# Kernel optimization log

Hardware: AMD Instinct MI355X
Metric: run time of the kernel (lower is better)

Reference implementation:

```python
import jax, jax.numpy as jnp
import numpy as np

B, S, D = 4, 4096, 64


def setup_inputs() -> dict:
    key = jax.random.key(0)
    ks = jax.random.split(key, 12)
    sc = 1.0 / np.sqrt(D)
    return {
        "q": jax.random.normal(ks[0], (B, S, D), jnp.float32),
        "k": jax.random.normal(ks[1], (B, S, D), jnp.float32),
        "v": jax.random.normal(ks[2], (B, S, D), jnp.float32),
        "attn_mask": jnp.ones((1, 1, 1), jnp.float32),
        "Wq": jax.random.normal(ks[3], (D, D), jnp.float32) * sc,
        "bq": jax.random.normal(ks[4], (D,), jnp.float32) * 0.01,
        "Wk": jax.random.normal(ks[5], (D, D), jnp.float32) * sc,
        "bk": jax.random.normal(ks[6], (D,), jnp.float32) * 0.01,
        "Wv": jax.random.normal(ks[7], (D, D), jnp.float32) * sc,
        "bv": jax.random.normal(ks[8], (D,), jnp.float32) * 0.01,
        "qw": jax.random.normal(ks[9], (1, 1, D), jnp.float32),
        "kw": jax.random.normal(ks[10], (1, 1, D), jnp.float32),
    }


def reference(q, k, v, attn_mask, Wq, bq, Wk, bk, Wv, bv, qw, kw):
    d = q.shape[-1]
    # Linear projections (torch Linear: x @ W.T + b)
    qp = q @ Wq.T + bq                      # (B,S,D)
    kp = k @ Wk.T + bk                      # (B,S,D)
    # learned per-feature elementwise weighting + 1/d scaling
    qwd = (qw * qp) / d                     # (B,S,D)
    kwd = (kw * kp) / d                     # (B,S,D)
    scores = jnp.einsum("bsd,btd->bst", qwd, kwd) + attn_mask  # (B,S,S)
    attn = jax.nn.softmax(scores, axis=-1)
    vp = v @ Wv.T + bv                      # (B,S,D)
    return jnp.einsum("bst,btd->bsd", attn, vp)
```

## Files before the change

### kernel.cpp

```cpp
#include <hip/hip_runtime.h>
#include <hip/hip_bf16.h>

typedef __attribute__((ext_vector_type(8)))  short    s16x8;
typedef __attribute__((ext_vector_type(16))) float    f32x16;
typedef __attribute__((ext_vector_type(4)))  unsigned u32x4;

#define NB 4
#define NS 4096
#define ND 64
#define NTOK (NB*NS)
#define PERB (NS*ND)

static __device__ __forceinline__ unsigned cvt_pk_bf16(float lo, float hi) {
    unsigned r;
    asm("v_cvt_pk_bf16_f32 %0, %1, %2" : "=v"(r) : "v"(lo), "v"(hi));
    return r;
}
static __device__ __forceinline__ float exp2_fast(float x) {
    float r;
    asm("v_exp_f32 %0, %1" : "=v"(r) : "v"(x));
    return r;
}
static __device__ __forceinline__ short f2bf_s(float x) {
    __hip_bfloat16 h = __float2bfloat16(x);
    return (short)__builtin_bit_cast(unsigned short, h);
}

__global__ __launch_bounds__(512) void proj_kernel(
    const float* __restrict__ q, const float* __restrict__ k, const float* __restrict__ v,
    const float* __restrict__ Wq, const float* __restrict__ bq,
    const float* __restrict__ Wk, const float* __restrict__ bk,
    const float* __restrict__ Wv, const float* __restrict__ bv,
    const float* __restrict__ qw, const float* __restrict__ kw,
    __hip_bfloat16* __restrict__ qf, __hip_bfloat16* __restrict__ kf,
    __hip_bfloat16* __restrict__ vf)
{
    const int which = blockIdx.y;
    const int wv    = __builtin_amdgcn_readfirstlane(threadIdx.x >> 6);
    const int lane  = threadIdx.x & 63;
    const int row   = blockIdx.x * 64 + lane;
    const float* X    = (which == 0) ? q  : (which == 1) ? k  : v;
    const float* W    = (which == 0) ? Wq : (which == 1) ? Wk : Wv;
    const float* bias = (which == 0) ? bq : (which == 1) ? bk : bv;

    float x[64];
    const float4* xr = (const float4*)(X + (size_t)row * ND);
    #pragma unroll
    for (int i = 0; i < 16; ++i) ((float4*)x)[i] = xr[i];

    float acc8[8];
    #pragma unroll
    for (int dd = 0; dd < 8; ++dd) {
        const float* wr = W + (8*wv + dd) * ND;
        float s = 0.f;
        #pragma unroll
        for (int i = 0; i < 64; ++i) s += x[i] * wr[i];
        acc8[dd] = s + bias[8*wv + dd];
    }

    const int b = row >> 12, t = row & (NS - 1);

    if (which == 2) {
        const size_t base = (size_t)b*PERB + (size_t)(t >> 6)*4096
                          + ((t >> 4) & 3)*512 + ((t >> 3) & 1)*256 + (t & 7)
                          + (wv >> 2)*2048;
        #pragma unroll
        for (int dd = 0; dd < 8; ++dd)
            vf[base + (8*(wv & 3) + dd)*8] = __float2bfloat16(acc8[dd]);
    } else {
        const float* sc = (which == 0) ? qw : kw;
        const float extra = (which == 0) ? 1.44269504088896f : 1.0f;
        s16x8 vch;
        #pragma unroll
        for (int j = 0; j < 8; ++j)
            vch[j] = f2bf_s(acc8[j] * sc[8*wv + j] * 0.015625f * extra);
        __hip_bfloat16* dst = ((which == 0) ? qf : kf)
            + (size_t)b*PERB + (size_t)(t >> 5)*2048 + wv*256 + (t & 31)*8;
        *(s16x8*)dst = vch;
    }
}

__global__ __launch_bounds__(64, 4) void attn_kernel(
    const __hip_bfloat16* __restrict__ qf, const __hip_bfloat16* __restrict__ kf,
    const __hip_bfloat16* __restrict__ vf,
    float* __restrict__ opart, float* __restrict__ lpart,
    float* __restrict__ outdirect, int nsplit)
{
    const int lane = threadIdx.x;
    const int r31 = lane & 31, hi = lane >> 5;
    const int bid = blockIdx.x;
    const int b     = bid & 3;
    const int qwi   = (bid >> 2) & 127;
    const int split = bid >> 9;

    const __hip_bfloat16* qb = qf + (size_t)b*PERB;
    const __hip_bfloat16* kb = kf + (size_t)b*PERB;
    const __hip_bfloat16* vb = vf + (size_t)b*PERB;

    const __hip_bfloat16* qr = qb + (size_t)qwi*2048 + hi*256 + r31*8;
    s16x8 bQ[4];
    #pragma unroll
    for (int c = 0; c < 4; ++c) bQ[c] = *(const s16x8*)(qr + c*512);

    f32x16 O0 = (f32x16)0.f, O1 = (f32x16)0.f;
    float l = 0.f;

    const int span  = NS / nsplit;
    const int tbeg  = split * span;
    const int iters = span >> 6;

    for (int it = 0; it < iters; ++it) {
        const int tb = tbeg + (it << 6);

        const __hip_bfloat16* kbase = kb + (size_t)(tb >> 5)*2048 + hi*256 + r31*8;
        f32x16 s0 = (f32x16)0.f, s1 = (f32x16)0.f;
        #pragma unroll
        for (int c = 0; c < 4; ++c) {
            s16x8 a0 = *(const s16x8*)(kbase + c*512);
            s16x8 a1 = *(const s16x8*)(kbase + 2048 + c*512);
            s0 = __builtin_amdgcn_mfma_f32_32x32x16_bf16(a0, bQ[c], s0, 0, 0, 0);
            s1 = __builtin_amdgcn_mfma_f32_32x32x16_bf16(a1, bQ[c], s1, 0, 0, 0);
        }

        #pragma unroll
        for (int r = 0; r < 16; ++r) { s0[r] = exp2_fast(s0[r]); s1[r] = exp2_fast(s1[r]); }
        float t0 = ((s0[0]+s0[1])+(s0[2]+s0[3])) + ((s0[4]+s0[5])+(s0[6]+s0[7]));
        float t1 = ((s0[8]+s0[9])+(s0[10]+s0[11])) + ((s0[12]+s0[13])+(s0[14]+s0[15]));
        float t2 = ((s1[0]+s1[1])+(s1[2]+s1[3])) + ((s1[4]+s1[5])+(s1[6]+s1[7]));
        float t3 = ((s1[8]+s1[9])+(s1[10]+s1[11])) + ((s1[12]+s1[13])+(s1[14]+s1[15]));
        float rs = (t0 + t1) + (t2 + t3);
        rs += __shfl_xor(rs, 32);
        l += rs;

        unsigned pw0[2][4], pw1[2][4];
        #pragma unroll
        for (int u = 0; u < 4; ++u) {
            pw0[0][u] = cvt_pk_bf16(s0[4*u],   s0[4*u+1]);
            pw1[0][u] = cvt_pk_bf16(s0[4*u+2], s0[4*u+3]);
            pw0[1][u] = cvt_pk_bf16(s1[4*u],   s1[4*u+1]);
            pw1[1][u] = cvt_pk_bf16(s1[4*u+2], s1[4*u+3]);
        }

        const __hip_bfloat16* vbase = vb + (size_t)(tb >> 6)*4096 + hi*256 + r31*8;
        #pragma unroll
        for (int ks = 0; ks < 4; ++ks) {
            const int tl = ks >> 1, k1 = ks & 1;
            unsigned x0 = pw0[tl][2*k1], y0 = pw0[tl][2*k1 + 1];
            unsigned x1 = pw1[tl][2*k1], y1 = pw1[tl][2*k1 + 1];
            asm("v_permlane32_swap_b32 %0, %1" : "+v"(x0), "+v"(y0));
            asm("v_permlane32_swap_b32 %0, %1" : "+v"(x1), "+v"(y1));
            u32x4 fv = {x0, x1, y0, y1};
            s16x8 bP = __builtin_bit_cast(s16x8, fv);
            s16x8 a0 = *(const s16x8*)(vbase + ks*512);
            s16x8 a1 = *(const s16x8*)(vbase + 2048 + ks*512);
            O0 = __builtin_amdgcn_mfma_f32_32x32x16_bf16(a0, bP, O0, 0, 0, 0);
            O1 = __builtin_amdgcn_mfma_f32_32x32x16_bf16(a1, bP, O1, 0, 0, 0);
        }
    }

    const int qrow = qwi * 32 + r31;
    const size_t gq = (size_t)b*NS + qrow;
    if (outdirect) {
        const float invl = 1.f / l;
        float* orow = outdirect + gq * ND;
        #pragma unroll
        for (int u = 0; u < 4; ++u) {
            const int d0 = 8*u + 4*hi;
            float4 w0v = {O0[4*u]*invl, O0[4*u+1]*invl, O0[4*u+2]*invl, O0[4*u+3]*invl};
            *(float4*)(orow + d0) = w0v;
            float4 w1v = {O1[4*u]*invl, O1[4*u+1]*invl, O1[4*u+2]*invl, O1[4*u+3]*invl};
            *(float4*)(orow + d0 + 32) = w1v;
        }
    } else {
        float* prow = opart + ((size_t)split*NTOK + gq) * ND;
        #pragma unroll
        for (int u = 0; u < 4; ++u) {
            const int d0 = 8*u + 4*hi;
            float4 w0v = {O0[4*u], O0[4*u+1], O0[4*u+2], O0[4*u+3]};
            *(float4*)(prow + d0) = w0v;
            float4 w1v = {O1[4*u], O1[4*u+1], O1[4*u+2], O1[4*u+3]};
            *(float4*)(prow + d0 + 32) = w1v;
        }
        if (lane < 32) lpart[(size_t)split*NTOK + gq] = l;
    }
}

__global__ __launch_bounds__(256) void combine_kernel(
    const float* __restrict__ opart, const float* __restrict__ lpart,
    float* __restrict__ out, int nsplit)
{
    const int tid = threadIdx.x;
    const int r = blockIdx.x * 16 + (tid >> 4);
    const int c = (tid & 15) * 4;
    float L = 0.f;
    float4 acc = {0.f, 0.f, 0.f, 0.f};
    #pragma unroll
    for (int s = 0; s < 8; ++s) {
        if (s >= nsplit) break;
        L += lpart[(size_t)s*NTOK + r];
        float4 o = *(const float4*)(opart + ((size_t)s*NTOK + r)*ND + c);
        acc.x += o.x; acc.y += o.y; acc.z += o.z; acc.w += o.w;
    }
    const float inv = 1.f / L;
    float4 res = {acc.x*inv, acc.y*inv, acc.z*inv, acc.w*inv};
    *(float4*)(out + (size_t)r*ND + c) = res;
}

extern "C" void kernel_launch(void* const* d_in, const int* in_sizes, int n_in,
                              void* d_out, int out_size, void* d_ws, size_t ws_size,
                              hipStream_t stream) {
    (void)in_sizes; (void)n_in; (void)out_size;
    const float* q  = (const float*)d_in[0];
    const float* k  = (const float*)d_in[1];
    const float* v  = (const float*)d_in[2];
    const float* Wq = (const float*)d_in[4];
    const float* bq = (const float*)d_in[5];
    const float* Wk = (const float*)d_in[6];
    const float* bk = (const float*)d_in[7];
    const float* Wv = (const float*)d_in[8];
    const float* bv = (const float*)d_in[9];
    const float* qw = (const float*)d_in[10];
    const float* kw = (const float*)d_in[11];

    __hip_bfloat16* qfb = (__hip_bfloat16*)d_ws;
    __hip_bfloat16* kfb = qfb + (size_t)NTOK*ND;
    __hip_bfloat16* vfb = kfb + (size_t)NTOK*ND;
    float* rest = (float*)(vfb + (size_t)NTOK*ND);

    auto need = [](int s) {
        return (size_t)NTOK*ND*2*3 + (size_t)s*NTOK*(ND*4 + 4);
    };
    const int nsplit = (ws_size >= need(8)) ? 8
                     : (ws_size >= need(4)) ? 4
                     : (ws_size >= need(2)) ? 2 : 1;

    float* opart = rest;
    float* lp = opart + (size_t)nsplit*NTOK*ND;

    proj_kernel<<<dim3(256, 3), 512, 0, stream>>>(q, k, v, Wq, bq, Wk, bk, Wv, bv,
                                                  qw, kw, qfb, kfb, vfb);
    attn_kernel<<<dim3(512*nsplit), 64, 0, stream>>>(
        qfb, kfb, vfb, opart, lp,
        (nsplit == 1) ? (float*)d_out : nullptr, nsplit);
    if (nsplit > 1)
        combine_kernel<<<dim3(NTOK/16), 256, 0, stream>>>(opart, lp,
                                                          (float*)d_out, nsplit);
}
```

Measured before the change: 125.4 us.

## Compute input projections with bf16 MFMA instead of scalar FP32 dot products

The projection kernel now converts each 32-row tile of inputs and the weight matrix to bf16 and computes the 64x64 linear layer with 32x32x16 MFMA instructions in a single wavefront. Bias, per-feature scale and output layout swizzles are applied from the MFMA accumulator layout. This replaces the scalar FP32 loop that had each wave recompute 8 output columns per row. Inputs and weights are rounded to bf16 before the matmul, which adds some error compared with the FP32 projection, and the index mapping for the swizzled outputs had to be rewritten.

```diff
diff --git a/kernel.cpp b/kernel.cpp
--- a/kernel.cpp
+++ b/kernel.cpp
@@ -2,8 +2,10 @@
 #include <hip/hip_bf16.h>
 
 typedef __attribute__((ext_vector_type(8)))  short    s16x8;
+typedef __attribute__((ext_vector_type(4)))  short    s16x4;
 typedef __attribute__((ext_vector_type(16))) float    f32x16;
 typedef __attribute__((ext_vector_type(4)))  unsigned u32x4;
+typedef __attribute__((ext_vector_type(2)))  unsigned u32x2;
 
 #define NB 4
 #define NS 4096
@@ -21,12 +23,8 @@
     asm("v_exp_f32 %0, %1" : "=v"(r) : "v"(x));
     return r;
 }
-static __device__ __forceinline__ short f2bf_s(float x) {
-    __hip_bfloat16 h = __float2bfloat16(x);
-    return (short)__builtin_bit_cast(unsigned short, h);
-}
-
-__global__ __launch_bounds__(512) void proj_kernel(
+
+__global__ __launch_bounds__(64) void proj_kernel(
     const float* __restrict__ q, const float* __restrict__ k, const float* __restrict__ v,
     const float* __restrict__ Wq, const float* __restrict__ bq,
     const float* __restrict__ Wk, const float* __restrict__ bk,
@@ -36,47 +34,82 @@
     __hip_bfloat16* __restrict__ vf)
 {
     const int which = blockIdx.y;
-    const int wv    = __builtin_amdgcn_readfirstlane(threadIdx.x >> 6);
-    const int lane  = threadIdx.x & 63;
-    const int row   = blockIdx.x * 64 + lane;
+    const int lane = threadIdx.x;
+    const int r31 = lane & 31, hi = lane >> 5;
+    const int bx = blockIdx.x;
     const float* X    = (which == 0) ? q  : (which == 1) ? k  : v;
     const float* W    = (which == 0) ? Wq : (which == 1) ? Wk : Wv;
     const float* bias = (which == 0) ? bq : (which == 1) ? bk : bv;
 
-    float x[64];
-    const float4* xr = (const float4*)(X + (size_t)row * ND);
-    #pragma unroll
-    for (int i = 0; i < 16; ++i) ((float4*)x)[i] = xr[i];
-
-    float acc8[8];
-    #pragma unroll
-    for (int dd = 0; dd < 8; ++dd) {
-        const float* wr = W + (8*wv + dd) * ND;
-        float s = 0.f;
-        #pragma unroll
-        for (int i = 0; i < 64; ++i) s += x[i] * wr[i];
-        acc8[dd] = s + bias[8*wv + dd];
-    }
-
-    const int b = row >> 12, t = row & (NS - 1);
+    const float* xrow = X + ((size_t)bx*32 + r31) * ND + 8*hi;
+    s16x8 xf[4];
+    #pragma unroll
+    for (int c = 0; c < 4; ++c) {
+        float4 f0 = *(const float4*)(xrow + 16*c);
+        float4 f1 = *(const float4*)(xrow + 16*c + 4);
+        u32x4 u = { cvt_pk_bf16(f0.x, f0.y), cvt_pk_bf16(f0.z, f0.w),
+                    cvt_pk_bf16(f1.x, f1.y), cvt_pk_bf16(f1.z, f1.w) };
+        xf[c] = __builtin_bit_cast(s16x8, u);
+    }
+    s16x8 wf[2][4];
+    #pragma unroll
+    for (int dt = 0; dt < 2; ++dt) {
+        const float* wrow = W + (size_t)(32*dt + r31) * ND + 8*hi;
+        #pragma unroll
+        for (int c = 0; c < 4; ++c) {
+            float4 f0 = *(const float4*)(wrow + 16*c);
+            float4 f1 = *(const float4*)(wrow + 16*c + 4);
+            u32x4 u = { cvt_pk_bf16(f0.x, f0.y), cvt_pk_bf16(f0.z, f0.w),
+                        cvt_pk_bf16(f1.x, f1.y), cvt_pk_bf16(f1.z, f1.w) };
+            wf[dt][c] = __builtin_bit_cast(s16x8, u);
+        }
+    }
+
+    f32x16 acc0 = (f32x16)0.f, acc1 = (f32x16)0.f;
 
     if (which == 2) {
-        const size_t base = (size_t)b*PERB + (size_t)(t >> 6)*4096
-                          + ((t >> 4) & 3)*512 + ((t >> 3) & 1)*256 + (t & 7)
-                          + (wv >> 2)*2048;
-        #pragma unroll
-        for (int dd = 0; dd < 8; ++dd)
-            vf[base + (8*(wv & 3) + dd)*8] = __float2bfloat16(acc8[dd]);
+        #pragma unroll
+        for (int c = 0; c < 4; ++c) {
+            acc0 = __builtin_amdgcn_mfma_f32_32x32x16_bf16(xf[c], wf[0][c], acc0, 0, 0, 0);
+            acc1 = __builtin_amdgcn_mfma_f32_32x32x16_bf16(xf[c], wf[1][c], acc1, 0, 0, 0);
+        }
+        const float b0 = bias[r31], b1 = bias[32 + r31];
+        __hip_bfloat16* dst = vf + (size_t)(bx >> 1)*4096 + (bx & 1)*1024
+                                 + r31*8 + 4*hi;
+        #pragma unroll
+        for (int g = 0; g < 4; ++g) {
+            u32x2 p0 = { cvt_pk_bf16(acc0[4*g]   + b0, acc0[4*g+1] + b0),
+                         cvt_pk_bf16(acc0[4*g+2] + b0, acc0[4*g+3] + b0) };
+            *(s16x4*)(dst + (g >> 1)*512 + (g & 1)*256) = __builtin_bit_cast(s16x4, p0);
+            u32x2 p1 = { cvt_pk_bf16(acc1[4*g]   + b1, acc1[4*g+1] + b1),
+                         cvt_pk_bf16(acc1[4*g+2] + b1, acc1[4*g+3] + b1) };
+            *(s16x4*)(dst + 2048 + (g >> 1)*512 + (g & 1)*256) = __builtin_bit_cast(s16x4, p1);
+        }
     } else {
+        #pragma unroll
+        for (int c = 0; c < 4; ++c) {
+            acc0 = __builtin_amdgcn_mfma_f32_32x32x16_bf16(wf[0][c], xf[c], acc0, 0, 0, 0);
+            acc1 = __builtin_amdgcn_mfma_f32_32x32x16_bf16(wf[1][c], xf[c], acc1, 0, 0, 0);
+        }
         const float* sc = (which == 0) ? qw : kw;
-        const float extra = (which == 0) ? 1.44269504088896f : 1.0f;
-        s16x8 vch;
-        #pragma unroll
-        for (int j = 0; j < 8; ++j)
-            vch[j] = f2bf_s(acc8[j] * sc[8*wv + j] * 0.015625f * extra);
-        __hip_bfloat16* dst = ((which == 0) ? qf : kf)
-            + (size_t)b*PERB + (size_t)(t >> 5)*2048 + wv*256 + (t & 31)*8;
-        *(s16x8*)dst = vch;
+        const float cf = (which == 0) ? (0.015625f * 1.44269504088896f) : 0.015625f;
+        __hip_bfloat16* dst = ((which == 0) ? qf : kf) + (size_t)bx*2048 + r31*8 + 4*hi;
+        #pragma unroll
+        for (int dt = 0; dt < 2; ++dt) {
+            const f32x16 acc = dt ? acc1 : acc0;
+            #pragma unroll
+            for (int g = 0; g < 4; ++g) {
+                const int dbase = 32*dt + 8*g + 4*hi;
+                float4 b4 = *(const float4*)(bias + dbase);
+                float4 s4 = *(const float4*)(sc + dbase);
+                float v0 = (acc[4*g+0] + b4.x) * (s4.x * cf);
+                float v1 = (acc[4*g+1] + b4.y) * (s4.y * cf);
+                float v2 = (acc[4*g+2] + b4.z) * (s4.z * cf);
+                float v3 = (acc[4*g+3] + b4.w) * (s4.w * cf);
+                u32x2 p = { cvt_pk_bf16(v0, v1), cvt_pk_bf16(v2, v3) };
+                *(s16x4*)(dst + (4*dt + g)*256) = __builtin_bit_cast(s16x4, p);
+            }
+        }
     }
 }
 
@@ -237,8 +270,8 @@
     float* opart = rest;
     float* lp = opart + (size_t)nsplit*NTOK*ND;
 
-    proj_kernel<<<dim3(256, 3), 512, 0, stream>>>(q, k, v, Wq, bq, Wk, bk, Wv, bv,
-                                                  qw, kw, qfb, kfb, vfb);
+    proj_kernel<<<dim3(512, 3), 64, 0, stream>>>(q, k, v, Wq, bq, Wk, bk, Wv, bv,
+                                                 qw, kw, qfb, kfb, vfb);
     attn_kernel<<<dim3(512*nsplit), 64, 0, stream>>>(
         qfb, kfb, vfb, opart, lp,
         (nsplit == 1) ? (float*)d_out : nullptr, nsplit);
```

New measurement: 115.7 us. 7.7% less time.
